# Kernel optimization log

Measured on AMD Instinct MI355X. Metric: run time of the kernel, lower is better.

The kernel has to match this reference:

```python
import jax, jax.numpy as jnp
import numpy as np

B, S, DIN = 2, 2048, 1024
H = 16
DK = 1024   # dim_key_query_all
DV = 1024   # dim_value_all
DOUT = 1024
HEAD_SIZE = DK / H  # attention_head_size (float division in source)
LN_EPS = 1e-5


def setup_inputs() -> dict:
    key = jax.random.key(0)
    ks = jax.random.split(key, 12)
    s_in = 1.0 / np.sqrt(DIN)
    s_dv = 1.0 / np.sqrt(DV)
    return {
        "hidden_states": jax.random.normal(ks[0], (B, S, DIN), jnp.float32),
        "Wq": jax.random.uniform(ks[1], (DK, DIN), jnp.float32, -s_in, s_in),
        "Wk": jax.random.uniform(ks[2], (DK, DIN), jnp.float32, -s_in, s_in),
        "Wcb": jax.random.uniform(ks[3], (H, DIN), jnp.float32, -s_in, s_in),
        "Wv": jax.random.uniform(ks[4], (DV, DIN), jnp.float32, -s_in, s_in),
        "bv": jax.random.uniform(ks[5], (DV,), jnp.float32, -s_in, s_in),
        "mixing": 0.2 * jax.random.normal(ks[6], (H, DK), jnp.float32),
        "Wd": jax.random.uniform(ks[7], (DOUT, DV), jnp.float32, -s_dv, s_dv),
        "bd": jax.random.uniform(ks[8], (DOUT,), jnp.float32, -s_dv, s_dv),
        "gamma": jnp.ones((DV,), jnp.float32),
        "beta": jnp.zeros((DV,), jnp.float32),
    }


def reference(hidden_states, Wq, Wk, Wcb, Wv, bv, mixing, Wd, bd, gamma, beta):
    x = hidden_states  # [B, S, DIN]; self-attention: from == to
    q = jnp.einsum('bsd,kd->bsk', x, Wq)  # [B,S,DK]
    k = jnp.einsum('bsd,kd->bsk', x, Wk)  # [B,S,DK]
    # scores[b,h,i,j] = sum_c q[b,i,c]*mixing[h,c]*k[b,j,c]
    scores = jnp.einsum('bic,hc,bjc->bhij', q, mixing, k)
    cb = jnp.einsum('bjd,hd->bhj', x, Wcb)  # content bias [B,H,S]
    scores = scores + cb[:, :, None, :]
    scores = scores / jnp.sqrt(jnp.asarray(HEAD_SIZE, scores.dtype))
    probs = jax.nn.softmax(scores, axis=-1)  # dropout p=0.0 -> identity
    v = jnp.einsum('bsd,vd->bsv', x, Wv) + bv  # [B,S,DV]
    v = v.reshape(B, S, H, DV // H)
    ctx = jnp.einsum('bhij,bjhv->bihv', probs, v).reshape(B, S, DV)
    out = jnp.einsum('bsv,ov->bso', ctx, Wd) + bd
    res = x + out
    mu = jnp.mean(res, axis=-1, keepdims=True)
    var = jnp.var(res, axis=-1, keepdims=True)
    out = (res - mu) * jax.lax.rsqrt(var + LN_EPS) * gamma + beta
    return (out,)
```

## Files before the change

kernel.cpp:

```cpp
#include <hip/hip_runtime.h>
#include <cstddef>
#include <cstdint>

#define B_    2
#define S_    2048
#define DIN_  1024
#define H_    16
#define DK_   1024
#define DV_   1024
#define DH_   64
#define DOUT_ 1024
#define M_    (B_ * S_)

typedef __attribute__((ext_vector_type(8)))  short short8;
typedef __attribute__((ext_vector_type(4)))  float float4v;
typedef __attribute__((ext_vector_type(16))) float float16v;
typedef _Float16 half8v __attribute__((ext_vector_type(8)));

__device__ __forceinline__ float bf16s_to_f(short s) {
  union { unsigned int u; float f; } cv;
  cv.u = ((unsigned int)(unsigned short)s) << 16;
  return cv.f;
}
__device__ __forceinline__ short f_to_bf16s(float f) {
  union { float f; unsigned int u; } cv;
  cv.f = f;
  unsigned int u = cv.u + 0x7FFFu + ((cv.u >> 16) & 1u);
  return (short)(u >> 16);
}
__device__ __forceinline__ short f_to_f16s(float f) {
  union { _Float16 h; short s; } cv;
  cv.h = (_Float16)f;
  return cv.s;
}
__device__ __forceinline__ unsigned pkrtz_u32(float a, float b) {
  union { __fp16 __attribute__((ext_vector_type(2))) h2; unsigned u; } cv;
  cv.h2 = __builtin_amdgcn_cvt_pkrtz(a, b);
  return cv.u;
}
__device__ __forceinline__ void gll16(const void* g, void* l) {
  __builtin_amdgcn_global_load_lds(
      (const __attribute__((address_space(1))) unsigned int*)g,
      (__attribute__((address_space(3))) unsigned int*)l, 16, 0, 0);
}

__global__ __launch_bounds__(256) void cast_kernel(const float* __restrict__ in,
                                                   short* __restrict__ out, int n4) {
  int i = blockIdx.x * 256 + threadIdx.x;
  if (i >= n4) return;
  float4 v = ((const float4*)in)[i];
  union { ushort4 u; short s[4]; } o;
  o.s[0] = f_to_bf16s(v.x); o.s[1] = f_to_bf16s(v.y);
  o.s[2] = f_to_bf16s(v.z); o.s[3] = f_to_bf16s(v.w);
  ((ushort4*)out)[i] = o.u;
}

__global__ __launch_bounds__(256) void cb_kernel(const float* __restrict__ x,
                                                 const float* __restrict__ Wcb,
                                                 float* __restrict__ CBs) {
  __shared__ float xs[DIN_];
  const int row = blockIdx.x;
  const int tid = threadIdx.x;
  #pragma unroll
  for (int it = 0; it < 4; ++it)
    xs[tid + it * 256] = x[(size_t)row * DIN_ + tid + it * 256];
  __syncthreads();
  const int lane = tid & 63, w = tid >> 6;
  const float SC = 0.125f * 1.44269504088896f;
  #pragma unroll
  for (int hh = 0; hh < 4; ++hh) {
    const int hidx = w * 4 + hh;
    float p = 0.f;
    for (int c = lane; c < DIN_; c += 64)
      p += xs[c] * Wcb[(size_t)hidx * DIN_ + c];
    #pragma unroll
    for (int mk = 1; mk < 64; mk <<= 1) p += __shfl_xor(p, mk);
    if (lane == 0) {
      const int bb = row / S_, ss = row % S_;
      CBs[((size_t)bb * H_ + hidx) * S_ + ss] = p * SC;
    }
  }
}

__global__ __launch_bounds__(256, 4) void gemm_nt(
    const short* __restrict__ A, const short* __restrict__ Bw,
    const float* __restrict__ bias, const float* __restrict__ resid,
    short* __restrict__ outb, float* __restrict__ outf, int mode) {
  const int KD = 1024, ND = 1024;
  __shared__ __align__(16) short As[64 * 128];
  __shared__ __align__(16) short Bs[64 * 128];
  const int tid  = threadIdx.x;
  const int lane = tid & 63;
  const int w    = tid >> 6;
  const int quad = lane >> 4;
  const int l16  = lane & 15;
  const int m0   = blockIdx.y * 64;
  const int n0   = blockIdx.x * 64;
  const int wm   = (w >> 1) * 32;
  const int wn   = (w & 1) * 32;

  const int drow = lane >> 4;
  const int dp   = lane & 15;

  const float4v zero = {0.f, 0.f, 0.f, 0.f};
  float4v acc[2][2];
  acc[0][0] = zero; acc[0][1] = zero; acc[1][0] = zero; acc[1][1] = zero;

  for (int k0 = 0; k0 < KD; k0 += 128) {
    __syncthreads();
    #pragma unroll
    for (int cc = 0; cc < 4; ++cc) {
      const int n = w * 4 + cc;
      const int r = 4 * n + drow;
      const int l = dp ^ (r & 15);
      gll16(A  + (size_t)(m0 + r) * KD + k0 + l * 8, &As[n * 512]);
      gll16(Bw + (size_t)(n0 + r) * KD + k0 + l * 8, &Bs[n * 512]);
    }
    __syncthreads();
    #pragma unroll
    for (int ks = 0; ks < 4; ++ks) {
      const int ca = ((ks * 4 + quad) ^ l16) * 8;
      short8 af0 = *(short8*)&As[(wm + l16) * 128 + ca];
      short8 af1 = *(short8*)&As[(wm + 16 + l16) * 128 + ca];
      short8 bg0 = *(short8*)&Bs[(wn + l16) * 128 + ca];
      short8 bg1 = *(short8*)&Bs[(wn + 16 + l16) * 128 + ca];
      acc[0][0] = __builtin_amdgcn_mfma_f32_16x16x32_bf16(af0, bg0, acc[0][0], 0, 0, 0);
      acc[0][1] = __builtin_amdgcn_mfma_f32_16x16x32_bf16(af0, bg1, acc[0][1], 0, 0, 0);
      acc[1][0] = __builtin_amdgcn_mfma_f32_16x16x32_bf16(af1, bg0, acc[1][0], 0, 0, 0);
      acc[1][1] = __builtin_amdgcn_mfma_f32_16x16x32_bf16(af1, bg1, acc[1][1], 0, 0, 0);
    }
  }

  #pragma unroll
  for (int mt = 0; mt < 2; ++mt)
    #pragma unroll
    for (int nt = 0; nt < 2; ++nt)
      #pragma unroll
      for (int r = 0; r < 4; ++r) {
        int row = m0 + wm + mt * 16 + quad * 4 + r;
        int col = n0 + wn + nt * 16 + l16;
        float v = acc[mt][nt][r];
        if (mode == 1 || mode == 5) v += bias[col];
        if (mode == 2)
          outf[(size_t)row * ND + col] = v + bias[col] + resid[(size_t)row * ND + col];
        else if (mode == 5) {
          int bb = row >> 11, ss = row & 2047;
          outb[((size_t)bb * DV_ + col) * S_ + ss] = f_to_f16s(v);
        } else if (mode == 6) {
          short* dst = outb + ((col >> 10) ? (size_t)M_ * 1024 : 0) +
                       (size_t)row * 1024 + (col & 1023);
          *dst = f_to_f16s(v);
        } else if (mode == 4)
          outb[(size_t)row * ND + col] = f_to_f16s(v);
        else
          outb[(size_t)row * ND + col] = f_to_bf16s(v);
      }
}

__global__ __launch_bounds__(256, 2) void attn_kernel(
    const short* __restrict__ Qf, const short* __restrict__ Kf,
    const short* __restrict__ Vtf, const float* __restrict__ mixing,
    const float* __restrict__ CBs, short* __restrict__ ctxb) {
  __shared__ __align__(16) short KsF[3 * 128 * 64];
  __shared__ __align__(16) short Vt[64][136];
  __shared__ __align__(16) short mix_s[DK_];
  __shared__ float cb_s[128];

  const int tid  = threadIdx.x;
  const int lane = tid & 63;
  const int l32  = lane & 31;
  const int l1   = lane >> 5;
  const int w    = tid >> 6;

  const int F    = blockIdx.x;
  const int xcd  = F & 7, rest = F >> 3;
  const int b    = xcd >> 2;
  const int h    = (xcd & 3) * 4 + (rest & 3);
  const int i0   = (rest >> 2) * 128;

  const float SC = 0.125f * 1.44269504088896f;
  for (int c = tid; c < DK_; c += 256) {
    union { _Float16 h; short s; } cv;
    cv.h = (_Float16)(mixing[(size_t)h * DK_ + c] * SC);
    mix_s[c] = cv.s;
  }

  const int iq = i0 + w * 32 + l32;
  const short* qptr  = Qf + ((size_t)b * S_ + iq) * DK_;
  const short* kbase = Kf + (size_t)b * S_ * DK_;
  const short* vtb   = Vtf + ((size_t)b * DV_ + h * DH_) * S_;
  const float* cbp   = CBs + ((size_t)b * H_ + h) * S_;

  float16v accS[4], accO[2];
  #pragma unroll
  for (int g = 0; g < 2; ++g)
    #pragma unroll
    for (int r = 0; r < 16; ++r) accO[g][r] = 0.f;
  float m_run = -1e30f, l_run = 0.f;

  const int nrow = lane >> 3;
  const int dp8  = lane & 7;

  const int vrow = tid >> 2;
  const int vseg = (tid & 3) * 32;

  for (int j0 = 0; j0 < S_; j0 += 128) {
    short8 vreg[4];
    #pragma unroll
    for (int c = 0; c < 4; ++c)
      vreg[c] = *(const short8*)(vtb + (size_t)vrow * S_ + j0 + vseg + c * 8);
    float cbv = 0.f;
    if (tid < 128) cbv = cbp[j0 + tid];
    __syncthreads();
    #pragma unroll
    for (int c = 0; c < 4; ++c)
      *(short8*)&Vt[vrow][vseg + c * 8] = vreg[c];
    if (tid < 128) cb_s[tid] = cbv;

    #pragma unroll
    for (int cc = 0; cc < 4; ++cc) {
      const int n = w * 4 + cc;
      const int r = 8 * n + nrow;
      const int lchunk = dp8 ^ (r & 7);
      gll16(kbase + (size_t)(j0 + r) * DK_ + lchunk * 8, &KsF[n * 512]);
    }
    #pragma unroll
    for (int cc = 0; cc < 4; ++cc) {
      const int n = w * 4 + cc;
      const int r = 8 * n + nrow;
      const int lchunk = dp8 ^ (r & 7);
      gll16(kbase + (size_t)(j0 + r) * DK_ + 64 + lchunk * 8,
            &KsF[8192 + n * 512]);
    }
    half8v qcur[4], qnext[4];
    #pragma unroll
    for (int ks = 0; ks < 4; ++ks) {
      qcur[ks] = *(const half8v*)(qptr + ks * 16 + l1 * 8);
      qnext[ks] = qcur[ks];
    }

    #pragma unroll
    for (int f = 0; f < 4; ++f)
      #pragma unroll
      for (int r = 0; r < 16; ++r) accS[f][r] = 0.f;

    __builtin_amdgcn_sched_barrier(0);
    asm volatile("s_waitcnt vmcnt(8) lgkmcnt(0)" ::: "memory");
    __builtin_amdgcn_s_barrier();
    __builtin_amdgcn_sched_barrier(0);

    int rd = 0;
    for (int t = 0; t < 16; ++t) {
      if (t < 14) {
        int wr = rd + 2; if (wr >= 3) wr -= 3;
        #pragma unroll
        for (int cc = 0; cc < 4; ++cc) {
          const int n = w * 4 + cc;
          const int r = 8 * n + nrow;
          const int lchunk = dp8 ^ (r & 7);
          gll16(kbase + (size_t)(j0 + r) * DK_ + (t + 2) * 64 + lchunk * 8,
                &KsF[wr * 8192 + n * 512]);
        }
      }
      if (t < 15) {
        #pragma unroll
        for (int ks = 0; ks < 4; ++ks)
          qnext[ks] = *(const half8v*)(qptr + (t + 1) * 64 + ks * 16 + l1 * 8);
      }
      const short* kb = &KsF[rd * 8192];
      __builtin_amdgcn_s_setprio(1);
      #pragma unroll
      for (int ks = 0; ks < 4; ++ks) {
        half8v mf = *(half8v*)&mix_s[t * 64 + ks * 16 + l1 * 8];
        half8v qm = qcur[ks] * mf;
        const int poff = (((2 * ks + l1) ^ (l32 & 7)) * 8) + l32 * 64;
        #pragma unroll
        for (int f = 0; f < 4; ++f) {
          half8v af = *(half8v*)&kb[f * 2048 + poff];
          accS[f] = __builtin_amdgcn_mfma_f32_32x32x16_f16(af, qm, accS[f], 0, 0, 0);
        }
      }
      __builtin_amdgcn_s_setprio(0);
      #pragma unroll
      for (int ks = 0; ks < 4; ++ks) qcur[ks] = qnext[ks];
      if (t < 15) {
        __builtin_amdgcn_sched_barrier(0);
        if (t < 14) asm volatile("s_waitcnt vmcnt(8)" ::: "memory");
        else        asm volatile("s_waitcnt vmcnt(4)" ::: "memory");
        __builtin_amdgcn_s_barrier();
        __builtin_amdgcn_sched_barrier(0);
      }
      rd = (rd + 1 == 3) ? 0 : rd + 1;
    }

    float tmax = -1e30f;
    #pragma unroll
    for (int f = 0; f < 4; ++f)
      #pragma unroll
      for (int q = 0; q < 4; ++q) {
        float4 cbq = *(float4*)&cb_s[f * 32 + q * 8 + l1 * 4];
        #pragma unroll
        for (int c = 0; c < 4; ++c) {
          accS[f][4 * q + c] += ((const float*)&cbq)[c];
          tmax = fmaxf(tmax, accS[f][4 * q + c]);
        }
      }
    tmax = fmaxf(tmax, __shfl_xor(tmax, 32));
    const float mnew = fmaxf(m_run, tmax);
    const float alpha = exp2f(m_run - mnew);
    float tsum = 0.f;
    #pragma unroll
    for (int f = 0; f < 4; ++f)
      #pragma unroll
      for (int r = 0; r < 16; ++r) {
        float pv = exp2f(accS[f][r] - mnew);
        accS[f][r] = pv;
        tsum += pv;
      }
    tsum += __shfl_xor(tsum, 32);
    l_run = l_run * alpha + tsum;
    m_run = mnew;
    #pragma unroll
    for (int g = 0; g < 2; ++g)
      #pragma unroll
      for (int r = 0; r < 16; ++r) accO[g][r] *= alpha;

    #pragma unroll
    for (int cpv = 0; cpv < 8; ++cpv) {
      const int t = cpv & 1, fp = cpv >> 1;
      float xo[4], yo[4], lo[4], hi[4];
      #pragma unroll
      for (int c = 0; c < 4; ++c) {
        xo[c] = __shfl_xor(accS[fp][8 * t + c], 32);
        yo[c] = __shfl_xor(accS[fp][8 * t + 4 + c], 32);
      }
      #pragma unroll
      for (int c = 0; c < 4; ++c) {
        lo[c] = l1 ? yo[c] : accS[fp][8 * t + c];
        hi[c] = l1 ? accS[fp][8 * t + 4 + c] : xo[c];
      }
      union { half8v v; unsigned u[4]; } pb;
      pb.u[0] = pkrtz_u32(lo[0], lo[1]);
      pb.u[1] = pkrtz_u32(lo[2], lo[3]);
      pb.u[2] = pkrtz_u32(hi[0], hi[1]);
      pb.u[3] = pkrtz_u32(hi[2], hi[3]);
      #pragma unroll
      for (int g = 0; g < 2; ++g) {
        half8v vf = *(half8v*)&Vt[g * 32 + l32][cpv * 16 + l1 * 8];
        accO[g] = __builtin_amdgcn_mfma_f32_32x32x16_f16(vf, pb.v, accO[g], 0, 0, 0);
      }
    }
  }

  const float rl = 1.0f / l_run;
  short* cbase = ctxb + ((size_t)b * S_ + iq) * DV_ + h * DH_;
  #pragma unroll
  for (int g = 0; g < 2; ++g)
    #pragma unroll
    for (int q = 0; q < 4; ++q) {
      const int dv = g * 32 + 8 * q + 4 * l1;
      union { ushort4 u4; short s[4]; } ov;
      #pragma unroll
      for (int r = 0; r < 4; ++r)
        ov.s[r] = f_to_bf16s(accO[g][4 * q + r] * rl);
      *(ushort4*)(cbase + dv) = ov.u4;
    }
}

__global__ __launch_bounds__(256) void ln_kernel(float* __restrict__ out,
                                                 const float* __restrict__ gamma,
                                                 const float* __restrict__ beta) {
  __shared__ float red[8];
  const int row = blockIdx.x;
  const int tid = threadIdx.x;
  float* p = out + (size_t)row * DOUT_;
  float4 v = ((const float4*)p)[tid];
  float s = v.x + v.y + v.z + v.w;
  #pragma unroll
  for (int mk = 1; mk < 64; mk <<= 1) s += __shfl_xor(s, mk);
  if ((tid & 63) == 0) red[tid >> 6] = s;
  __syncthreads();
  const float mean = (red[0] + red[1] + red[2] + red[3]) * (1.0f / 1024.0f);
  const float d0 = v.x - mean, d1 = v.y - mean, d2 = v.z - mean, d3 = v.w - mean;
  float sq = d0 * d0 + d1 * d1 + d2 * d2 + d3 * d3;
  #pragma unroll
  for (int mk = 1; mk < 64; mk <<= 1) sq += __shfl_xor(sq, mk);
  if ((tid & 63) == 0) red[4 + (tid >> 6)] = sq;
  __syncthreads();
  const float var = (red[4] + red[5] + red[6] + red[7]) * (1.0f / 1024.0f);
  const float rstd = rsqrtf(var + 1e-5f);
  float4 g = ((const float4*)gamma)[tid];
  float4 bt = ((const float4*)beta)[tid];
  float4 o;
  o.x = d0 * rstd * g.x + bt.x;
  o.y = d1 * rstd * g.y + bt.y;
  o.z = d2 * rstd * g.z + bt.z;
  o.w = d3 * rstd * g.w + bt.w;
  ((float4*)p)[tid] = o;
}

extern "C" void kernel_launch(void* const* d_in, const int* in_sizes, int n_in,
                              void* d_out, int out_size, void* d_ws, size_t ws_size,
                              hipStream_t stream) {
  (void)in_sizes; (void)n_in; (void)out_size; (void)ws_size;
  const float* x      = (const float*)d_in[0];
  const float* Wq     = (const float*)d_in[1];
  const float* Wk     = (const float*)d_in[2];
  const float* Wcb    = (const float*)d_in[3];
  const float* Wv     = (const float*)d_in[4];
  const float* bv     = (const float*)d_in[5];
  const float* mixing = (const float*)d_in[6];
  const float* Wd     = (const float*)d_in[7];
  const float* bd     = (const float*)d_in[8];
  const float* gamma  = (const float*)d_in[9];
  const float* beta   = (const float*)d_in[10];
  float* out = (float*)d_out;

  short* p = (short*)d_ws;
  short* xb   = p; p += (size_t)M_ * DIN_;
  short* Qf   = p; p += (size_t)M_ * DK_;
  short* Kf   = p; p += (size_t)M_ * DK_;
  short* Vtf  = p; p += (size_t)B_ * DV_ * S_;
  short* ctxb = p; p += (size_t)M_ * DV_;
  short* Wqb  = p; p += (size_t)DK_ * DIN_;
  short* Wkb  = p; p += (size_t)DK_ * DIN_;
  short* Wvb  = p; p += (size_t)DV_ * DIN_;
  short* Wdb  = p; p += (size_t)DOUT_ * DV_;
  float* CBs  = (float*)p;
  (void)Kf; (void)Wkb;

  cast_kernel<<<dim3(M_ * DIN_ / 1024), 256, 0, stream>>>(x, xb, M_ * DIN_ / 4);
  cast_kernel<<<dim3(DK_ * DIN_ / 1024), 256, 0, stream>>>(Wq, Wqb, DK_ * DIN_ / 4);
  cast_kernel<<<dim3(DK_ * DIN_ / 1024), 256, 0, stream>>>(Wk, Wkb, DK_ * DIN_ / 4);
  cast_kernel<<<dim3(DV_ * DIN_ / 1024), 256, 0, stream>>>(Wv, Wvb, DV_ * DIN_ / 4);
  cast_kernel<<<dim3(DOUT_ * DV_ / 1024), 256, 0, stream>>>(Wd, Wdb, DOUT_ * DV_ / 4);
  cb_kernel<<<dim3(M_), 256, 0, stream>>>(x, Wcb, CBs);

  dim3 gqk(2048 / 64, M_ / 64);
  gemm_nt<<<gqk, 256, 0, stream>>>(xb, Wqb, nullptr, nullptr, Qf, nullptr, 6);
  dim3 gg(DOUT_ / 64, M_ / 64);
  gemm_nt<<<gg, 256, 0, stream>>>(xb, Wvb, bv, nullptr, Vtf, nullptr, 5);

  attn_kernel<<<dim3(512), 256, 0, stream>>>(Qf, Kf, Vtf, mixing, CBs, ctxb);

  gemm_nt<<<gg, 256, 0, stream>>>(ctxb, Wdb, bd, x, nullptr, out, 2);
  ln_kernel<<<dim3(M_), 256, 0, stream>>>(out, gamma, beta);
}
```

Measured before the change: 617.0 us.

## Flatten attention key-tile loop into one continuous K prefetch pipeline

Merges the outer key-tile loop and the inner 16-step DK loop into one 256-step loop. The triple-buffered K prefetch now runs across tile boundaries instead of draining and restarting at every tile. V tile loads are issued at step 0 and stored to LDS at step 4. The content bias is read straight from global memory instead of being staged through shared memory. This is meant to remove the per-tile pipeline bubble and the extra __syncthreads, in exchange for hand-tuned vmcnt wait counts that must match the new load ordering exactly.

```diff
diff --git a/kernel.cpp b/kernel.cpp
--- a/kernel.cpp
+++ b/kernel.cpp
@@ -164,7 +164,6 @@
   __shared__ __align__(16) short KsF[3 * 128 * 64];
   __shared__ __align__(16) short Vt[64][136];
   __shared__ __align__(16) short mix_s[DK_];
-  __shared__ float cb_s[128];
 
   const int tid  = threadIdx.x;
   const int lane = tid & 63;
@@ -193,6 +192,10 @@
 
   float16v accS[4], accO[2];
   #pragma unroll
+  for (int f = 0; f < 4; ++f)
+    #pragma unroll
+    for (int r = 0; r < 16; ++r) accS[f][r] = 0.f;
+  #pragma unroll
   for (int g = 0; g < 2; ++g)
     #pragma unroll
     for (int r = 0; r < 16; ++r) accO[g][r] = 0.f;
@@ -204,152 +207,155 @@
   const int vrow = tid >> 2;
   const int vseg = (tid & 3) * 32;
 
-  for (int j0 = 0; j0 < S_; j0 += 128) {
-    short8 vreg[4];
-    #pragma unroll
-    for (int c = 0; c < 4; ++c)
-      vreg[c] = *(const short8*)(vtb + (size_t)vrow * S_ + j0 + vseg + c * 8);
-    float cbv = 0.f;
-    if (tid < 128) cbv = cbp[j0 + tid];
-    __syncthreads();
-    #pragma unroll
-    for (int c = 0; c < 4; ++c)
-      *(short8*)&Vt[vrow][vseg + c * 8] = vreg[c];
-    if (tid < 128) cb_s[tid] = cbv;
-
-    #pragma unroll
-    for (int cc = 0; cc < 4; ++cc) {
-      const int n = w * 4 + cc;
-      const int r = 8 * n + nrow;
-      const int lchunk = dp8 ^ (r & 7);
-      gll16(kbase + (size_t)(j0 + r) * DK_ + lchunk * 8, &KsF[n * 512]);
-    }
-    #pragma unroll
-    for (int cc = 0; cc < 4; ++cc) {
-      const int n = w * 4 + cc;
-      const int r = 8 * n + nrow;
-      const int lchunk = dp8 ^ (r & 7);
-      gll16(kbase + (size_t)(j0 + r) * DK_ + 64 + lchunk * 8,
-            &KsF[8192 + n * 512]);
-    }
-    half8v qcur[4], qnext[4];
+  #pragma unroll
+  for (int cc = 0; cc < 4; ++cc) {
+    const int n = w * 4 + cc;
+    const int r = 8 * n + nrow;
+    const int lchunk = dp8 ^ (r & 7);
+    gll16(kbase + (size_t)r * DK_ + lchunk * 8, &KsF[n * 512]);
+  }
+  #pragma unroll
+  for (int cc = 0; cc < 4; ++cc) {
+    const int n = w * 4 + cc;
+    const int r = 8 * n + nrow;
+    const int lchunk = dp8 ^ (r & 7);
+    gll16(kbase + (size_t)r * DK_ + 64 + lchunk * 8, &KsF[8192 + n * 512]);
+  }
+  half8v qcur[4], qnext[4];
+  #pragma unroll
+  for (int ks = 0; ks < 4; ++ks) {
+    qcur[ks] = *(const half8v*)(qptr + ks * 16 + l1 * 8);
+    qnext[ks] = qcur[ks];
+  }
+  __builtin_amdgcn_sched_barrier(0);
+  asm volatile("s_waitcnt vmcnt(8) lgkmcnt(0)" ::: "memory");
+  __builtin_amdgcn_s_barrier();
+  __builtin_amdgcn_sched_barrier(0);
+
+  int rd = 0;
+  short8 vreg[4];
+
+  for (int s = 0; s < 256; ++s) {
+    const int jt = s >> 4, t = s & 15;
+
+    if (s < 254) {
+      const int s2 = s + 2;
+      const int jt2 = s2 >> 4, t2 = s2 & 15;
+      int wr = rd + 2; if (wr >= 3) wr -= 3;
+      #pragma unroll
+      for (int cc = 0; cc < 4; ++cc) {
+        const int n = w * 4 + cc;
+        const int r = 8 * n + nrow;
+        const int lchunk = dp8 ^ (r & 7);
+        gll16(kbase + (size_t)(jt2 * 128 + r) * DK_ + t2 * 64 + lchunk * 8,
+              &KsF[wr * 8192 + n * 512]);
+      }
+    }
+    if (s < 255) {
+      const int t1 = (s + 1) & 15;
+      #pragma unroll
+      for (int ks = 0; ks < 4; ++ks)
+        qnext[ks] = *(const half8v*)(qptr + t1 * 64 + ks * 16 + l1 * 8);
+    }
+    if (t == 0) {
+      #pragma unroll
+      for (int c = 0; c < 4; ++c)
+        vreg[c] = *(const short8*)(vtb + (size_t)vrow * S_ + jt * 128 + vseg + c * 8);
+    } else if (t == 4) {
+      #pragma unroll
+      for (int c = 0; c < 4; ++c)
+        *(short8*)&Vt[vrow][vseg + c * 8] = vreg[c];
+    }
+    const short* kb = &KsF[rd * 8192];
+    __builtin_amdgcn_s_setprio(1);
     #pragma unroll
     for (int ks = 0; ks < 4; ++ks) {
-      qcur[ks] = *(const half8v*)(qptr + ks * 16 + l1 * 8);
-      qnext[ks] = qcur[ks];
-    }
-
-    #pragma unroll
-    for (int f = 0; f < 4; ++f)
-      #pragma unroll
-      for (int r = 0; r < 16; ++r) accS[f][r] = 0.f;
-
-    __builtin_amdgcn_sched_barrier(0);
-    asm volatile("s_waitcnt vmcnt(8) lgkmcnt(0)" ::: "memory");
-    __builtin_amdgcn_s_barrier();
-    __builtin_amdgcn_sched_barrier(0);
-
-    int rd = 0;
-    for (int t = 0; t < 16; ++t) {
-      if (t < 14) {
-        int wr = rd + 2; if (wr >= 3) wr -= 3;
-        #pragma unroll
-        for (int cc = 0; cc < 4; ++cc) {
-          const int n = w * 4 + cc;
-          const int r = 8 * n + nrow;
-          const int lchunk = dp8 ^ (r & 7);
-          gll16(kbase + (size_t)(j0 + r) * DK_ + (t + 2) * 64 + lchunk * 8,
-                &KsF[wr * 8192 + n * 512]);
+      half8v mf = *(half8v*)&mix_s[t * 64 + ks * 16 + l1 * 8];
+      half8v qm = qcur[ks] * mf;
+      const int poff = (((2 * ks + l1) ^ (l32 & 7)) * 8) + l32 * 64;
+      #pragma unroll
+      for (int f = 0; f < 4; ++f) {
+        half8v af = *(half8v*)&kb[f * 2048 + poff];
+        accS[f] = __builtin_amdgcn_mfma_f32_32x32x16_f16(af, qm, accS[f], 0, 0, 0);
+      }
+    }
+    __builtin_amdgcn_s_setprio(0);
+    #pragma unroll
+    for (int ks = 0; ks < 4; ++ks) qcur[ks] = qnext[ks];
+
+    if (t == 15) {
+      float tmax = -1e30f;
+      #pragma unroll
+      for (int f = 0; f < 4; ++f)
+        #pragma unroll
+        for (int q = 0; q < 4; ++q) {
+          float4 cbq = *(const float4*)(cbp + jt * 128 + f * 32 + q * 8 + l1 * 4);
+          #pragma unroll
+          for (int c = 0; c < 4; ++c) {
+            accS[f][4 * q + c] += ((const float*)&cbq)[c];
+            tmax = fmaxf(tmax, accS[f][4 * q + c]);
+          }
+        }
+      tmax = fmaxf(tmax, __shfl_xor(tmax, 32));
+      const float mnew = fmaxf(m_run, tmax);
+      const float alpha = exp2f(m_run - mnew);
+      float tsum = 0.f;
+      #pragma unroll
+      for (int f = 0; f < 4; ++f)
+        #pragma unroll
+        for (int r = 0; r < 16; ++r) {
+          float pv = exp2f(accS[f][r] - mnew);
+          accS[f][r] = pv;
+          tsum += pv;
+        }
+      tsum += __shfl_xor(tsum, 32);
+      l_run = l_run * alpha + tsum;
+      m_run = mnew;
+      #pragma unroll
+      for (int g = 0; g < 2; ++g)
+        #pragma unroll
+        for (int r = 0; r < 16; ++r) accO[g][r] *= alpha;
+
+      #pragma unroll
+      for (int cpv = 0; cpv < 8; ++cpv) {
+        const int tt = cpv & 1, fp = cpv >> 1;
+        float xo[4], yo[4], lo[4], hi[4];
+        #pragma unroll
+        for (int c = 0; c < 4; ++c) {
+          xo[c] = __shfl_xor(accS[fp][8 * tt + c], 32);
+          yo[c] = __shfl_xor(accS[fp][8 * tt + 4 + c], 32);
+        }
+        #pragma unroll
+        for (int c = 0; c < 4; ++c) {
+          lo[c] = l1 ? yo[c] : accS[fp][8 * tt + c];
+          hi[c] = l1 ? accS[fp][8 * tt + 4 + c] : xo[c];
+        }
+        union { half8v v; unsigned u[4]; } pb;
+        pb.u[0] = pkrtz_u32(lo[0], lo[1]);
+        pb.u[1] = pkrtz_u32(lo[2], lo[3]);
+        pb.u[2] = pkrtz_u32(hi[0], hi[1]);
+        pb.u[3] = pkrtz_u32(hi[2], hi[3]);
+        #pragma unroll
+        for (int g = 0; g < 2; ++g) {
+          half8v vf = *(half8v*)&Vt[g * 32 + l32][cpv * 16 + l1 * 8];
+          accO[g] = __builtin_amdgcn_mfma_f32_32x32x16_f16(vf, pb.v, accO[g], 0, 0, 0);
         }
       }
-      if (t < 15) {
-        #pragma unroll
-        for (int ks = 0; ks < 4; ++ks)
-          qnext[ks] = *(const half8v*)(qptr + (t + 1) * 64 + ks * 16 + l1 * 8);
-      }
-      const short* kb = &KsF[rd * 8192];
-      __builtin_amdgcn_s_setprio(1);
-      #pragma unroll
-      for (int ks = 0; ks < 4; ++ks) {
-        half8v mf = *(half8v*)&mix_s[t * 64 + ks * 16 + l1 * 8];
-        half8v qm = qcur[ks] * mf;
-        const int poff = (((2 * ks + l1) ^ (l32 & 7)) * 8) + l32 * 64;
-        #pragma unroll
-        for (int f = 0; f < 4; ++f) {
-          half8v af = *(half8v*)&kb[f * 2048 + poff];
-          accS[f] = __builtin_amdgcn_mfma_f32_32x32x16_f16(af, qm, accS[f], 0, 0, 0);
-        }
-      }
-      __builtin_amdgcn_s_setprio(0);
-      #pragma unroll
-      for (int ks = 0; ks < 4; ++ks) qcur[ks] = qnext[ks];
-      if (t < 15) {
-        __builtin_amdgcn_sched_barrier(0);
-        if (t < 14) asm volatile("s_waitcnt vmcnt(8)" ::: "memory");
-        else        asm volatile("s_waitcnt vmcnt(4)" ::: "memory");
-        __builtin_amdgcn_s_barrier();
-        __builtin_amdgcn_sched_barrier(0);
-      }
-      rd = (rd + 1 == 3) ? 0 : rd + 1;
-    }
-
-    float tmax = -1e30f;
-    #pragma unroll
-    for (int f = 0; f < 4; ++f)
-      #pragma unroll
-      for (int q = 0; q < 4; ++q) {
-        float4 cbq = *(float4*)&cb_s[f * 32 + q * 8 + l1 * 4];
-        #pragma unroll
-        for (int c = 0; c < 4; ++c) {
-          accS[f][4 * q + c] += ((const float*)&cbq)[c];
-          tmax = fmaxf(tmax, accS[f][4 * q + c]);
-        }
-      }
-    tmax = fmaxf(tmax, __shfl_xor(tmax, 32));
-    const float mnew = fmaxf(m_run, tmax);
-    const float alpha = exp2f(m_run - mnew);
-    float tsum = 0.f;
-    #pragma unroll
-    for (int f = 0; f < 4; ++f)
-      #pragma unroll
-      for (int r = 0; r < 16; ++r) {
-        float pv = exp2f(accS[f][r] - mnew);
-        accS[f][r] = pv;
-        tsum += pv;
-      }
-    tsum += __shfl_xor(tsum, 32);
-    l_run = l_run * alpha + tsum;
-    m_run = mnew;
-    #pragma unroll
-    for (int g = 0; g < 2; ++g)
-      #pragma unroll
-      for (int r = 0; r < 16; ++r) accO[g][r] *= alpha;
-
-    #pragma unroll
-    for (int cpv = 0; cpv < 8; ++cpv) {
-      const int t = cpv & 1, fp = cpv >> 1;
-      float xo[4], yo[4], lo[4], hi[4];
-      #pragma unroll
-      for (int c = 0; c < 4; ++c) {
-        xo[c] = __shfl_xor(accS[fp][8 * t + c], 32);
-        yo[c] = __shfl_xor(accS[fp][8 * t + 4 + c], 32);
-      }
-      #pragma unroll
-      for (int c = 0; c < 4; ++c) {
-        lo[c] = l1 ? yo[c] : accS[fp][8 * t + c];
-        hi[c] = l1 ? accS[fp][8 * t + 4 + c] : xo[c];
-      }
-      union { half8v v; unsigned u[4]; } pb;
-      pb.u[0] = pkrtz_u32(lo[0], lo[1]);
-      pb.u[1] = pkrtz_u32(lo[2], lo[3]);
-      pb.u[2] = pkrtz_u32(hi[0], hi[1]);
-      pb.u[3] = pkrtz_u32(hi[2], hi[3]);
-      #pragma unroll
-      for (int g = 0; g < 2; ++g) {
-        half8v vf = *(half8v*)&Vt[g * 32 + l32][cpv * 16 + l1 * 8];
-        accO[g] = __builtin_amdgcn_mfma_f32_32x32x16_f16(vf, pb.v, accO[g], 0, 0, 0);
-      }
-    }
+      #pragma unroll
+      for (int f = 0; f < 4; ++f)
+        #pragma unroll
+        for (int r = 0; r < 16; ++r) accS[f][r] = 0.f;
+    }
+
+    if (s < 255) {
+      __builtin_amdgcn_sched_barrier(0);
+      if (t == 0)      asm volatile("s_waitcnt vmcnt(12)" ::: "memory");
+      else if (t == 4) asm volatile("s_waitcnt vmcnt(8) lgkmcnt(0)" ::: "memory");
+      else             asm volatile("s_waitcnt vmcnt(8)" ::: "memory");
+      __builtin_amdgcn_s_barrier();
+      __builtin_amdgcn_sched_barrier(0);
+    }
+    rd = (rd + 1 == 3) ? 0 : rd + 1;
   }
 
   const float rl = 1.0f / l_run;
```

Result: slower. 659.8 us (+6.9%).
